# Kernel tuning notes

Hardware: AMD Instinct MI355X
Metric: run time of the kernel (lower is better)

Reference implementation:

```python
import jax, jax.numpy as jnp
import numpy as np
from jax.scipy.special import erf

# synthetic covalent radii table (original imports `covalent_radii`, e.g. from ase)
COV_RADII = jnp.asarray(0.3 + 0.02 * np.arange(100), dtype=jnp.float32)

B_MOL = 1024   # molecules per batch
N_ATOM = 128   # atoms per molecule (equal-sized ragged batch, atoms sorted by molecule)
N_ELEM = 10


def setup_inputs() -> dict:
    key = jax.random.key(0)
    ks = jax.random.split(key, 6)
    N = B_MOL * N_ATOM
    return {
        "eneg": jax.random.normal(ks[0], (N, 1), jnp.float32),
        "positions": jax.random.normal(ks[1], (N, 3), jnp.float32) * 3.0,
        "node_attrs": jax.random.uniform(ks[2], (N, N_ELEM), jnp.float32),
        "hardness": jax.random.uniform(ks[3], (N_ELEM,), jnp.float32),
        "total_charge": jax.random.normal(ks[4], (B_MOL,), jnp.float32),
        "batch": jnp.repeat(jnp.arange(B_MOL), N_ATOM),          # sorted molecule ids
        "atomic_numbers": jax.random.randint(ks[5], (N,), 1, 90),
    }


def reference(eneg, positions, node_attrs, hardness, total_charge, batch, atomic_numbers):
    # atoms are sorted by molecule with equal molecule sizes, so the ragged
    # python loop of the original collapses to a batched [B, n, ...] computation.
    B = total_charge.shape[0]
    N = positions.shape[0]
    n = N // B
    sqrt_pi = jnp.sqrt(jnp.asarray(np.pi, jnp.float32))
    sqrt_2 = jnp.sqrt(jnp.asarray(2.0, jnp.float32))

    pos = positions.reshape(B, n, 3)
    Z = atomic_numbers.reshape(B, n)
    atom_idx = jnp.argmax(node_attrs, axis=1).reshape(B, n)

    r = COV_RADII[Z]                                     # [B, n]
    diag_vals = hardness[atom_idx] + 1.0 / (sqrt_pi * r)  # [B, n]
    sigma = jnp.square(r)                                # [B, n]
    gamma = jnp.sqrt(sigma[:, :, None] + sigma[:, None, :])  # [B, n, n]

    diff = pos[:, :, None, :] - pos[:, None, :, :]       # [B, n, n, 3]
    sq = jnp.sum(diff * diff, axis=-1)                   # [B, n, n]
    eye = jnp.eye(n, dtype=bool)
    dist = jnp.sqrt(jnp.where(eye, 1.0, sq))             # safe diag (overwritten below)

    A = erf(dist / (sqrt_2 * gamma)) / dist              # [B, n, n]
    A = jnp.where(eye, diag_vals[:, :, None], A)         # scatter hardness diagonal

    # augment with charge-conservation row/column of ones (corner = 1)
    A = jnp.concatenate([A, jnp.ones((B, n, 1), A.dtype)], axis=2)
    A = jnp.concatenate([A, jnp.ones((B, 1, n + 1), A.dtype)], axis=1)

    b = jnp.concatenate([-eneg.reshape(B, n, 1),
                         total_charge.reshape(B, 1, 1)], axis=1)  # [B, n+1, 1]

    x = jnp.linalg.solve(A, b)                           # batched small solves
    return x[:, :n, 0].reshape(-1)                       # partial charges, [N]
```

## Files before the change

### kernel.cpp

```cpp
#include <hip/hip_runtime.h>
#include <math.h>

#define NMOL  1024
#define N     128
#define NELEM 10
#define BLOCK 256
#define PW    8
#define NPAN  16
#define PSTR  12
#define USTR  132

typedef __attribute__((ext_vector_type(4))) float f4;


__global__ __launch_bounds__(BLOCK, 2) void ceq_solve_kernel(
    const float* __restrict__ eneg,
    const float* __restrict__ positions,
    const float* __restrict__ node_attrs,
    const float* __restrict__ hardness,
    const float* __restrict__ total_charge,
    const int*   __restrict__ atomic_numbers,
    float* __restrict__ out)
{
    __shared__ __align__(16) float P[2][N * PSTR];
    __shared__ __align__(16) float Up[2][PW * USTR];
    __shared__ __align__(16) float Ublk[2][NPAN][PW][PW];
    __shared__ float rhsY[2][N], rhsZ[2][N];
    __shared__ float sxY[2][N], sxZ[2][N];
    __shared__ float px[2][N], py[2][N], pz[2][N], sg[2][N], dgv[2][N];
    __shared__ float lamS[2];

    const int tid  = threadIdx.x;
    const int lane = tid & 63;
    const int wid  = tid >> 6;
    const int g    = tid >> 7;
    const int wv   = wid & 1;
    const int gt   = tid & 127;
    const int r0   = 2 * lane;
    const int r1   = r0 + 1;
    const int col0 = 64 * wv;
    const int mol  = 2 * blockIdx.x + g;
    const int base = mol * N;

    {
        const int i = gt;
        const int Z = atomic_numbers[base + i];
        const float rad = 0.3f + 0.02f * (float)Z;
        sg[g][i] = rad * rad;
        const float* na = node_attrs + (size_t)(base + i) * NELEM;
        float best = na[0]; int bi = 0;
        #pragma unroll
        for (int e = 1; e < NELEM; ++e) {
            float v = na[e];
            if (v > best) { best = v; bi = e; }
        }
        dgv[g][i] = hardness[bi] + 0.5641895835477563f / rad;
        const float* p = positions + (size_t)(base + i) * 3;
        px[g][i] = p[0]; py[g][i] = p[1]; pz[g][i] = p[2];
        rhsY[g][i] = -eneg[base + i];
        rhsZ[g][i] = 1.0f;
    }
    __syncthreads();

    f4 Ar0[16], Ar1[16];
    {
        const float x0 = px[g][r0], y0 = py[g][r0], z0 = pz[g][r0];
        const float s0 = sg[g][r0], d0 = dgv[g][r0];
        #pragma unroll
        for (int c = 0; c < 16; ++c) {
            f4 v0;
            #pragma unroll
            for (int e = 0; e < 4; ++e) {
                const int j = col0 + 4 * c + e;
                float a0;
                if (j == r0) a0 = d0;
                else {
                    const float dx = x0 - px[g][j], dy = y0 - py[g][j], dz = z0 - pz[g][j];
                    const float d = sqrtf(dx * dx + dy * dy + dz * dz);
                    a0 = erff(d / (1.4142135623730951f * sqrtf(s0 + sg[g][j]))) / d;
                }
                ((float*)&v0)[e] = a0;
            }
            Ar0[c] = v0;
        }
        const float x1 = px[g][r1], y1 = py[g][r1], z1 = pz[g][r1];
        const float s1 = sg[g][r1], d1 = dgv[g][r1];
        #pragma unroll
        for (int c = 0; c < 16; ++c) {
            f4 v1;
            #pragma unroll
            for (int e = 0; e < 4; ++e) {
                const int j = col0 + 4 * c + e;
                float a1;
                if (j == r1) a1 = d1;
                else {
                    const float dx = x1 - px[g][j], dy = y1 - py[g][j], dz = z1 - pz[g][j];
                    const float d = sqrtf(dx * dx + dy * dy + dz * dz);
                    a1 = erff(d / (1.4142135623730951f * sqrtf(s1 + sg[g][j]))) / d;
                }
                ((float*)&v1)[e] = a1;
            }
            Ar1[c] = v1;
        }
    }

    for (int p = 0; p < NPAN; ++p) {
        const int k0   = PW * p;
        const int gclo = 2 * p + 2;
        const int q    = p & 7;

        if (wv == (p >> 3) && lane >= 4 * p) {
            f4 a00, a01, a10, a11;
            switch (q) {
                case 0:  a00 = Ar0[0];  a01 = Ar0[1];  a10 = Ar1[0];  a11 = Ar1[1];  break;
                case 1:  a00 = Ar0[2];  a01 = Ar0[3];  a10 = Ar1[2];  a11 = Ar1[3];  break;
                case 2:  a00 = Ar0[4];  a01 = Ar0[5];  a10 = Ar1[4];  a11 = Ar1[5];  break;
                case 3:  a00 = Ar0[6];  a01 = Ar0[7];  a10 = Ar1[6];  a11 = Ar1[7];  break;
                case 4:  a00 = Ar0[8];  a01 = Ar0[9];  a10 = Ar1[8];  a11 = Ar1[9];  break;
                case 5:  a00 = Ar0[10]; a01 = Ar0[11]; a10 = Ar1[10]; a11 = Ar1[11]; break;
                case 6:  a00 = Ar0[12]; a01 = Ar0[13]; a10 = Ar1[12]; a11 = Ar1[13]; break;
                default: a00 = Ar0[14]; a01 = Ar0[15]; a10 = Ar1[14]; a11 = Ar1[15]; break;
            }
            *(f4*)&P[g][r0 * PSTR + 0] = a00; *(f4*)&P[g][r0 * PSTR + 4] = a01;
            *(f4*)&P[g][r1 * PSTR + 0] = a10; *(f4*)&P[g][r1 * PSTR + 4] = a11;
        }
        __syncthreads();

        if (wv == 0) {
            const int i0 = k0 + lane, i1 = i0 + 64;
            const bool v0 = i0 < N, v1 = i1 < N;
            float rg0[PW], rg1[PW];
            float rY0, rZ0, rY1, rZ1;
            if (v0) {
                f4 a = *(const f4*)&P[g][i0 * PSTR], b = *(const f4*)&P[g][i0 * PSTR + 4];
                rg0[0]=a.x; rg0[1]=a.y; rg0[2]=a.z; rg0[3]=a.w;
                rg0[4]=b.x; rg0[5]=b.y; rg0[6]=b.z; rg0[7]=b.w;
                rY0 = rhsY[g][i0]; rZ0 = rhsZ[g][i0];
            } else {
                #pragma unroll
                for (int j = 0; j < PW; ++j) rg0[j] = 0.0f;
                rY0 = 0.0f; rZ0 = 0.0f;
            }
            if (v1) {
                f4 a = *(const f4*)&P[g][i1 * PSTR], b = *(const f4*)&P[g][i1 * PSTR + 4];
                rg1[0]=a.x; rg1[1]=a.y; rg1[2]=a.z; rg1[3]=a.w;
                rg1[4]=b.x; rg1[5]=b.y; rg1[6]=b.z; rg1[7]=b.w;
                rY1 = rhsY[g][i1]; rZ1 = rhsZ[g][i1];
            } else {
                #pragma unroll
                for (int j = 0; j < PW; ++j) rg1[j] = 0.0f;
                rY1 = 0.0f; rZ1 = 0.0f;
            }
            #pragma unroll
            for (int kk = 0; kk < PW; ++kk) {
                float pr[PW];
                #pragma unroll
                for (int j = kk; j < PW; ++j) pr[j] = __shfl(rg0[j], kk);
                const float cY = __shfl(rY0, kk);
                const float cZ = __shfl(rZ0, kk);
                const float dinv = 1.0f / pr[kk];
                if (v0 && lane > kk) {
                    const float mult = rg0[kk] * dinv; rg0[kk] = mult;
                    #pragma unroll
                    for (int j = kk + 1; j < PW; ++j) rg0[j] -= mult * pr[j];
                    rY0 -= mult * cY; rZ0 -= mult * cZ;
                }
                if (v0 && lane >= PW) Up[g][kk * USTR + i0] = rg0[kk] * pr[kk];
                if (v1) {
                    const float mult = rg1[kk] * dinv; rg1[kk] = mult;
                    #pragma unroll
                    for (int j = kk + 1; j < PW; ++j) rg1[j] -= mult * pr[j];
                    rY1 -= mult * cY; rZ1 -= mult * cZ;
                    Up[g][kk * USTR + i1] = rg1[kk] * pr[kk];
                }
            }
            if (v0) {
                f4 a = { rg0[0], rg0[1], rg0[2], rg0[3] };
                f4 b = { rg0[4], rg0[5], rg0[6], rg0[7] };
                *(f4*)&P[g][i0 * PSTR] = a; *(f4*)&P[g][i0 * PSTR + 4] = b;
                rhsY[g][i0] = rY0; rhsZ[g][i0] = rZ0;
                if (lane < PW) {
                    *(f4*)&Ublk[g][p][lane][0] = a; *(f4*)&Ublk[g][p][lane][4] = b;
                }
            }
            if (v1) {
                f4 a = { rg1[0], rg1[1], rg1[2], rg1[3] };
                f4 b = { rg1[4], rg1[5], rg1[6], rg1[7] };
                *(f4*)&P[g][i1 * PSTR] = a; *(f4*)&P[g][i1 * PSTR + 4] = b;
                rhsY[g][i1] = rY1; rhsZ[g][i1] = rZ1;
            }
        }
        __syncthreads();

        if (lane >= 4 * p && lane < 4 * p + 4) {
            const int u0 = r0 - k0, u1 = u0 + 1;
            #pragma unroll
            for (int c = 0; c < 16; ++c) {
                const int gc = 16 * wv + c;
                if (gc >= gclo) {
                    Ar0[c] = *(const f4*)&Up[g][u0 * USTR + 4 * gc];
                    Ar1[c] = *(const f4*)&Up[g][u1 * USTR + 4 * gc];
                }
            }
        }
        const bool hasmat = (16 * wv + 15) >= gclo;
        if (hasmat && lane >= 4 * p + 4) {
            float lA0[PW], lA1[PW];
            {
                f4 a = *(const f4*)&P[g][r0 * PSTR], b = *(const f4*)&P[g][r0 * PSTR + 4];
                lA0[0]=a.x; lA0[1]=a.y; lA0[2]=a.z; lA0[3]=a.w;
                lA0[4]=b.x; lA0[5]=b.y; lA0[6]=b.z; lA0[7]=b.w;
                f4 c2 = *(const f4*)&P[g][r1 * PSTR], d2 = *(const f4*)&P[g][r1 * PSTR + 4];
                lA1[0]=c2.x; lA1[1]=c2.y; lA1[2]=c2.z; lA1[3]=c2.w;
                lA1[4]=d2.x; lA1[5]=d2.y; lA1[6]=d2.z; lA1[7]=d2.w;
            }
            #pragma unroll
            for (int c = 0; c < 16; ++c) {
                const int gc = 16 * wv + c;
                if (gc >= gclo) {
                    f4 acc0 = Ar0[c], acc1 = Ar1[c];
                    #pragma unroll
                    for (int u = 0; u < PW; ++u) {
                        const f4 uv = *(const f4*)&Up[g][u * USTR + 4 * gc];
                        acc0 -= uv * lA0[u];
                        acc1 -= uv * lA1[u];
                    }
                    Ar0[c] = acc0; Ar1[c] = acc1;
                }
            }
        }
        __syncthreads();
    }

    for (int pb = NPAN - 1; pb >= 0; --pb) {
        const int k0 = PW * pb;
        if (tid < 4) {
            const int gg = tid >> 1;
            float* rhs = (tid & 1) ? rhsZ[gg] : rhsY[gg];
            float* sx  = (tid & 1) ? sxZ[gg]  : sxY[gg];
            float x[PW];
            #pragma unroll
            for (int kk = PW - 1; kk >= 0; --kk) {
                float acc = rhs[k0 + kk];
                #pragma unroll
                for (int jj = kk + 1; jj < PW; ++jj) acc -= Ublk[gg][pb][kk][jj] * x[jj];
                x[kk] = acc / Ublk[gg][pb][kk][kk];
                sx[k0 + kk] = x[kk];
            }
        }
        __syncthreads();
        if (wv == (pb >> 3) && lane < 4 * pb) {
            f4 a00, a01, a10, a11;
            switch (pb & 7) {
                case 0:  a00 = Ar0[0];  a01 = Ar0[1];  a10 = Ar1[0];  a11 = Ar1[1];  break;
                case 1:  a00 = Ar0[2];  a01 = Ar0[3];  a10 = Ar1[2];  a11 = Ar1[3];  break;
                case 2:  a00 = Ar0[4];  a01 = Ar0[5];  a10 = Ar1[4];  a11 = Ar1[5];  break;
                case 3:  a00 = Ar0[6];  a01 = Ar0[7];  a10 = Ar1[6];  a11 = Ar1[7];  break;
                case 4:  a00 = Ar0[8];  a01 = Ar0[9];  a10 = Ar1[8];  a11 = Ar1[9];  break;
                case 5:  a00 = Ar0[10]; a01 = Ar0[11]; a10 = Ar1[10]; a11 = Ar1[11]; break;
                case 6:  a00 = Ar0[12]; a01 = Ar0[13]; a10 = Ar1[12]; a11 = Ar1[13]; break;
                default: a00 = Ar0[14]; a01 = Ar0[15]; a10 = Ar1[14]; a11 = Ar1[15]; break;
            }
            float yy0 = rhsY[g][r0], yy1 = rhsY[g][r1];
            float zz0 = rhsZ[g][r0], zz1 = rhsZ[g][r1];
            yy0 -= a00.x*sxY[g][k0]   + a00.y*sxY[g][k0+1] + a00.z*sxY[g][k0+2] + a00.w*sxY[g][k0+3]
                 + a01.x*sxY[g][k0+4] + a01.y*sxY[g][k0+5] + a01.z*sxY[g][k0+6] + a01.w*sxY[g][k0+7];
            yy1 -= a10.x*sxY[g][k0]   + a10.y*sxY[g][k0+1] + a10.z*sxY[g][k0+2] + a10.w*sxY[g][k0+3]
                 + a11.x*sxY[g][k0+4] + a11.y*sxY[g][k0+5] + a11.z*sxY[g][k0+6] + a11.w*sxY[g][k0+7];
            zz0 -= a00.x*sxZ[g][k0]   + a00.y*sxZ[g][k0+1] + a00.z*sxZ[g][k0+2] + a00.w*sxZ[g][k0+3]
                 + a01.x*sxZ[g][k0+4] + a01.y*sxZ[g][k0+5] + a01.z*sxZ[g][k0+6] + a01.w*sxZ[g][k0+7];
            zz1 -= a10.x*sxZ[g][k0]   + a10.y*sxZ[g][k0+1] + a10.z*sxZ[g][k0+2] + a10.w*sxZ[g][k0+3]
                 + a11.x*sxZ[g][k0+4] + a11.y*sxZ[g][k0+5] + a11.z*sxZ[g][k0+6] + a11.w*sxZ[g][k0+7];
            rhsY[g][r0] = yy0; rhsY[g][r1] = yy1;
            rhsZ[g][r0] = zz0; rhsZ[g][r1] = zz1;
        }
        __syncthreads();
    }

    if (wv == 0) {
        float vY = sxY[g][lane] + sxY[g][lane + 64];
        float vZ = sxZ[g][lane] + sxZ[g][lane + 64];
        #pragma unroll
        for (int off = 32; off; off >>= 1) {
            vY += __shfl_xor(vY, off);
            vZ += __shfl_xor(vZ, off);
        }
        if (lane == 0) lamS[g] = (vY - total_charge[mol]) / (vZ - 1.0f);
    }
    __syncthreads();
    out[base + gt] = sxY[g][gt] - lamS[g] * sxZ[g][gt];
}

extern "C" void kernel_launch(void* const* d_in, const int* in_sizes, int n_in,
                              void* d_out, int out_size, void* d_ws, size_t ws_size,
                              hipStream_t stream) {
    const float* eneg           = (const float*)d_in[0];
    const float* positions      = (const float*)d_in[1];
    const float* node_attrs     = (const float*)d_in[2];
    const float* hardness       = (const float*)d_in[3];
    const float* total_charge   = (const float*)d_in[4];
    const int*   atomic_numbers = (const int*)d_in[6];
    float* out = (float*)d_out;

    ceq_solve_kernel<<<NMOL / 2, BLOCK, 0, stream>>>(
        eneg, positions, node_attrs, hardness, total_charge, atomic_numbers, out);
}
```

Measured before the change: 223.0 us.

## Assign one molecule per 256-thread block with four waves sharing its columns

Each block now solves one molecule instead of two, and its four wavefronts each own 32 columns of the 128x128 matrix rather than two wavefronts owning 64. Each thread holds half as many matrix registers (8 f4 per row instead of 16), so launch bounds are raised to 4 blocks per CU and the grid doubles. The aim is more parallelism per molecule and higher occupancy, shortening the serial panel chain per block. In exchange, the panel-factor step still runs on one wave while the other three wait, and idle threads per molecule increase.

```diff
diff --git a/kernel.cpp b/kernel.cpp
--- a/kernel.cpp
+++ b/kernel.cpp
@@ -13,7 +13,7 @@
 typedef __attribute__((ext_vector_type(4))) float f4;
 
 
-__global__ __launch_bounds__(BLOCK, 2) void ceq_solve_kernel(
+__global__ __launch_bounds__(BLOCK, 4) void ceq_solve_kernel(
     const float* __restrict__ eneg,
     const float* __restrict__ positions,
     const float* __restrict__ node_attrs,
@@ -22,31 +22,28 @@
     const int*   __restrict__ atomic_numbers,
     float* __restrict__ out)
 {
-    __shared__ __align__(16) float P[2][N * PSTR];
-    __shared__ __align__(16) float Up[2][PW * USTR];
-    __shared__ __align__(16) float Ublk[2][NPAN][PW][PW];
-    __shared__ float rhsY[2][N], rhsZ[2][N];
-    __shared__ float sxY[2][N], sxZ[2][N];
-    __shared__ float px[2][N], py[2][N], pz[2][N], sg[2][N], dgv[2][N];
-    __shared__ float lamS[2];
+    __shared__ __align__(16) float P[N * PSTR];
+    __shared__ __align__(16) float Up[PW * USTR];
+    __shared__ __align__(16) float Ublk[NPAN][PW][PW];
+    __shared__ float rhsY[N], rhsZ[N];
+    __shared__ float sxY[N], sxZ[N];
+    __shared__ float px[N], py[N], pz[N], sg[N], dgv[N];
+    __shared__ float lamS;
 
     const int tid  = threadIdx.x;
     const int lane = tid & 63;
-    const int wid  = tid >> 6;
-    const int g    = tid >> 7;
-    const int wv   = wid & 1;
-    const int gt   = tid & 127;
+    const int wv   = tid >> 6;
     const int r0   = 2 * lane;
     const int r1   = r0 + 1;
-    const int col0 = 64 * wv;
-    const int mol  = 2 * blockIdx.x + g;
+    const int col0 = 32 * wv;
+    const int mol  = blockIdx.x;
     const int base = mol * N;
 
-    {
-        const int i = gt;
+    if (tid < N) {
+        const int i = tid;
         const int Z = atomic_numbers[base + i];
         const float rad = 0.3f + 0.02f * (float)Z;
-        sg[g][i] = rad * rad;
+        sg[i] = rad * rad;
         const float* na = node_attrs + (size_t)(base + i) * NELEM;
         float best = na[0]; int bi = 0;
         #pragma unroll
@@ -54,20 +51,20 @@
             float v = na[e];
             if (v > best) { best = v; bi = e; }
         }
-        dgv[g][i] = hardness[bi] + 0.5641895835477563f / rad;
+        dgv[i] = hardness[bi] + 0.5641895835477563f / rad;
         const float* p = positions + (size_t)(base + i) * 3;
-        px[g][i] = p[0]; py[g][i] = p[1]; pz[g][i] = p[2];
-        rhsY[g][i] = -eneg[base + i];
-        rhsZ[g][i] = 1.0f;
+        px[i] = p[0]; py[i] = p[1]; pz[i] = p[2];
+        rhsY[i] = -eneg[base + i];
+        rhsZ[i] = 1.0f;
     }
     __syncthreads();
 
-    f4 Ar0[16], Ar1[16];
+    f4 Ar0[8], Ar1[8];
     {
-        const float x0 = px[g][r0], y0 = py[g][r0], z0 = pz[g][r0];
-        const float s0 = sg[g][r0], d0 = dgv[g][r0];
-        #pragma unroll
-        for (int c = 0; c < 16; ++c) {
+        const float x0 = px[r0], y0 = py[r0], z0 = pz[r0];
+        const float s0 = sg[r0], d0 = dgv[r0];
+        #pragma unroll
+        for (int c = 0; c < 8; ++c) {
             f4 v0;
             #pragma unroll
             for (int e = 0; e < 4; ++e) {
@@ -75,18 +72,18 @@
                 float a0;
                 if (j == r0) a0 = d0;
                 else {
-                    const float dx = x0 - px[g][j], dy = y0 - py[g][j], dz = z0 - pz[g][j];
+                    const float dx = x0 - px[j], dy = y0 - py[j], dz = z0 - pz[j];
                     const float d = sqrtf(dx * dx + dy * dy + dz * dz);
-                    a0 = erff(d / (1.4142135623730951f * sqrtf(s0 + sg[g][j]))) / d;
+                    a0 = erff(d / (1.4142135623730951f * sqrtf(s0 + sg[j]))) / d;
                 }
                 ((float*)&v0)[e] = a0;
             }
             Ar0[c] = v0;
         }
-        const float x1 = px[g][r1], y1 = py[g][r1], z1 = pz[g][r1];
-        const float s1 = sg[g][r1], d1 = dgv[g][r1];
-        #pragma unroll
-        for (int c = 0; c < 16; ++c) {
+        const float x1 = px[r1], y1 = py[r1], z1 = pz[r1];
+        const float s1 = sg[r1], d1 = dgv[r1];
+        #pragma unroll
+        for (int c = 0; c < 8; ++c) {
             f4 v1;
             #pragma unroll
             for (int e = 0; e < 4; ++e) {
@@ -94,9 +91,9 @@
                 float a1;
                 if (j == r1) a1 = d1;
                 else {
-                    const float dx = x1 - px[g][j], dy = y1 - py[g][j], dz = z1 - pz[g][j];
+                    const float dx = x1 - px[j], dy = y1 - py[j], dz = z1 - pz[j];
                     const float d = sqrtf(dx * dx + dy * dy + dz * dz);
-                    a1 = erff(d / (1.4142135623730951f * sqrtf(s1 + sg[g][j]))) / d;
+                    a1 = erff(d / (1.4142135623730951f * sqrtf(s1 + sg[j]))) / d;
                 }
                 ((float*)&v1)[e] = a1;
             }
@@ -107,22 +104,18 @@
     for (int p = 0; p < NPAN; ++p) {
         const int k0   = PW * p;
         const int gclo = 2 * p + 2;
-        const int q    = p & 7;
-
-        if (wv == (p >> 3) && lane >= 4 * p) {
+        const int q    = p & 3;
+
+        if (wv == (p >> 2) && lane >= 4 * p) {
             f4 a00, a01, a10, a11;
             switch (q) {
-                case 0:  a00 = Ar0[0];  a01 = Ar0[1];  a10 = Ar1[0];  a11 = Ar1[1];  break;
-                case 1:  a00 = Ar0[2];  a01 = Ar0[3];  a10 = Ar1[2];  a11 = Ar1[3];  break;
-                case 2:  a00 = Ar0[4];  a01 = Ar0[5];  a10 = Ar1[4];  a11 = Ar1[5];  break;
-                case 3:  a00 = Ar0[6];  a01 = Ar0[7];  a10 = Ar1[6];  a11 = Ar1[7];  break;
-                case 4:  a00 = Ar0[8];  a01 = Ar0[9];  a10 = Ar1[8];  a11 = Ar1[9];  break;
-                case 5:  a00 = Ar0[10]; a01 = Ar0[11]; a10 = Ar1[10]; a11 = Ar1[11]; break;
-                case 6:  a00 = Ar0[12]; a01 = Ar0[13]; a10 = Ar1[12]; a11 = Ar1[13]; break;
-                default: a00 = Ar0[14]; a01 = Ar0[15]; a10 = Ar1[14]; a11 = Ar1[15]; break;
-            }
-            *(f4*)&P[g][r0 * PSTR + 0] = a00; *(f4*)&P[g][r0 * PSTR + 4] = a01;
-            *(f4*)&P[g][r1 * PSTR + 0] = a10; *(f4*)&P[g][r1 * PSTR + 4] = a11;
+                case 0:  a00 = Ar0[0]; a01 = Ar0[1]; a10 = Ar1[0]; a11 = Ar1[1]; break;
+                case 1:  a00 = Ar0[2]; a01 = Ar0[3]; a10 = Ar1[2]; a11 = Ar1[3]; break;
+                case 2:  a00 = Ar0[4]; a01 = Ar0[5]; a10 = Ar1[4]; a11 = Ar1[5]; break;
+                default: a00 = Ar0[6]; a01 = Ar0[7]; a10 = Ar1[6]; a11 = Ar1[7]; break;
+            }
+            *(f4*)&P[r0 * PSTR + 0] = a00; *(f4*)&P[r0 * PSTR + 4] = a01;
+            *(f4*)&P[r1 * PSTR + 0] = a10; *(f4*)&P[r1 * PSTR + 4] = a11;
         }
         __syncthreads();
 
@@ -132,20 +125,20 @@
             float rg0[PW], rg1[PW];
             float rY0, rZ0, rY1, rZ1;
             if (v0) {
-                f4 a = *(const f4*)&P[g][i0 * PSTR], b = *(const f4*)&P[g][i0 * PSTR + 4];
+                f4 a = *(const f4*)&P[i0 * PSTR], b = *(const f4*)&P[i0 * PSTR + 4];
                 rg0[0]=a.x; rg0[1]=a.y; rg0[2]=a.z; rg0[3]=a.w;
                 rg0[4]=b.x; rg0[5]=b.y; rg0[6]=b.z; rg0[7]=b.w;
-                rY0 = rhsY[g][i0]; rZ0 = rhsZ[g][i0];
+                rY0 = rhsY[i0]; rZ0 = rhsZ[i0];
             } else {
                 #pragma unroll
                 for (int j = 0; j < PW; ++j) rg0[j] = 0.0f;
                 rY0 = 0.0f; rZ0 = 0.0f;
             }
             if (v1) {
-                f4 a = *(const f4*)&P[g][i1 * PSTR], b = *(const f4*)&P[g][i1 * PSTR + 4];
+                f4 a = *(const f4*)&P[i1 * PSTR], b = *(const f4*)&P[i1 * PSTR + 4];
                 rg1[0]=a.x; rg1[1]=a.y; rg1[2]=a.z; rg1[3]=a.w;
                 rg1[4]=b.x; rg1[5]=b.y; rg1[6]=b.z; rg1[7]=b.w;
-                rY1 = rhsY[g][i1]; rZ1 = rhsZ[g][i1];
+                rY1 = rhsY[i1]; rZ1 = rhsZ[i1];
             } else {
                 #pragma unroll
                 for (int j = 0; j < PW; ++j) rg1[j] = 0.0f;
@@ -165,29 +158,29 @@
                     for (int j = kk + 1; j < PW; ++j) rg0[j] -= mult * pr[j];
                     rY0 -= mult * cY; rZ0 -= mult * cZ;
                 }
-                if (v0 && lane >= PW) Up[g][kk * USTR + i0] = rg0[kk] * pr[kk];
+                if (v0 && lane >= PW) Up[kk * USTR + i0] = rg0[kk] * pr[kk];
                 if (v1) {
                     const float mult = rg1[kk] * dinv; rg1[kk] = mult;
                     #pragma unroll
                     for (int j = kk + 1; j < PW; ++j) rg1[j] -= mult * pr[j];
                     rY1 -= mult * cY; rZ1 -= mult * cZ;
-                    Up[g][kk * USTR + i1] = rg1[kk] * pr[kk];
+                    Up[kk * USTR + i1] = rg1[kk] * pr[kk];
                 }
             }
             if (v0) {
                 f4 a = { rg0[0], rg0[1], rg0[2], rg0[3] };
                 f4 b = { rg0[4], rg0[5], rg0[6], rg0[7] };
-                *(f4*)&P[g][i0 * PSTR] = a; *(f4*)&P[g][i0 * PSTR + 4] = b;
-                rhsY[g][i0] = rY0; rhsZ[g][i0] = rZ0;
+                *(f4*)&P[i0 * PSTR] = a; *(f4*)&P[i0 * PSTR + 4] = b;
+                rhsY[i0] = rY0; rhsZ[i0] = rZ0;
                 if (lane < PW) {
-                    *(f4*)&Ublk[g][p][lane][0] = a; *(f4*)&Ublk[g][p][lane][4] = b;
+                    *(f4*)&Ublk[p][lane][0] = a; *(f4*)&Ublk[p][lane][4] = b;
                 }
             }
             if (v1) {
                 f4 a = { rg1[0], rg1[1], rg1[2], rg1[3] };
                 f4 b = { rg1[4], rg1[5], rg1[6], rg1[7] };
-                *(f4*)&P[g][i1 * PSTR] = a; *(f4*)&P[g][i1 * PSTR + 4] = b;
-                rhsY[g][i1] = rY1; rhsZ[g][i1] = rZ1;
+                *(f4*)&P[i1 * PSTR] = a; *(f4*)&P[i1 * PSTR + 4] = b;
+                rhsY[i1] = rY1; rhsZ[i1] = rZ1;
             }
         }
         __syncthreads();
@@ -195,33 +188,33 @@
         if (lane >= 4 * p && lane < 4 * p + 4) {
             const int u0 = r0 - k0, u1 = u0 + 1;
             #pragma unroll
-            for (int c = 0; c < 16; ++c) {
-                const int gc = 16 * wv + c;
+            for (int c = 0; c < 8; ++c) {
+                const int gc = 8 * wv + c;
                 if (gc >= gclo) {
-                    Ar0[c] = *(const f4*)&Up[g][u0 * USTR + 4 * gc];
-                    Ar1[c] = *(const f4*)&Up[g][u1 * USTR + 4 * gc];
-                }
-            }
-        }
-        const bool hasmat = (16 * wv + 15) >= gclo;
+                    Ar0[c] = *(const f4*)&Up[u0 * USTR + 4 * gc];
+                    Ar1[c] = *(const f4*)&Up[u1 * USTR + 4 * gc];
+                }
+            }
+        }
+        const bool hasmat = (8 * wv + 7) >= gclo;
         if (hasmat && lane >= 4 * p + 4) {
             float lA0[PW], lA1[PW];
             {
-                f4 a = *(const f4*)&P[g][r0 * PSTR], b = *(const f4*)&P[g][r0 * PSTR + 4];
+                f4 a = *(const f4*)&P[r0 * PSTR], b = *(const f4*)&P[r0 * PSTR + 4];
                 lA0[0]=a.x; lA0[1]=a.y; lA0[2]=a.z; lA0[3]=a.w;
                 lA0[4]=b.x; lA0[5]=b.y; lA0[6]=b.z; lA0[7]=b.w;
-                f4 c2 = *(const f4*)&P[g][r1 * PSTR], d2 = *(const f4*)&P[g][r1 * PSTR + 4];
+                f4 c2 = *(const f4*)&P[r1 * PSTR], d2 = *(const f4*)&P[r1 * PSTR + 4];
                 lA1[0]=c2.x; lA1[1]=c2.y; lA1[2]=c2.z; lA1[3]=c2.w;
                 lA1[4]=d2.x; lA1[5]=d2.y; lA1[6]=d2.z; lA1[7]=d2.w;
             }
             #pragma unroll
-            for (int c = 0; c < 16; ++c) {
-                const int gc = 16 * wv + c;
+            for (int c = 0; c < 8; ++c) {
+                const int gc = 8 * wv + c;
                 if (gc >= gclo) {
                     f4 acc0 = Ar0[c], acc1 = Ar1[c];
                     #pragma unroll
                     for (int u = 0; u < PW; ++u) {
-                        const f4 uv = *(const f4*)&Up[g][u * USTR + 4 * gc];
+                        const f4 uv = *(const f4*)&Up[u * USTR + 4 * gc];
                         acc0 -= uv * lA0[u];
                         acc1 -= uv * lA1[u];
                     }
@@ -234,61 +227,56 @@
 
     for (int pb = NPAN - 1; pb >= 0; --pb) {
         const int k0 = PW * pb;
-        if (tid < 4) {
-            const int gg = tid >> 1;
-            float* rhs = (tid & 1) ? rhsZ[gg] : rhsY[gg];
-            float* sx  = (tid & 1) ? sxZ[gg]  : sxY[gg];
+        if (tid < 2) {
+            float* rhs = tid ? rhsZ : rhsY;
+            float* sx  = tid ? sxZ  : sxY;
             float x[PW];
             #pragma unroll
             for (int kk = PW - 1; kk >= 0; --kk) {
                 float acc = rhs[k0 + kk];
                 #pragma unroll
-                for (int jj = kk + 1; jj < PW; ++jj) acc -= Ublk[gg][pb][kk][jj] * x[jj];
-                x[kk] = acc / Ublk[gg][pb][kk][kk];
+                for (int jj = kk + 1; jj < PW; ++jj) acc -= Ublk[pb][kk][jj] * x[jj];
+                x[kk] = acc / Ublk[pb][kk][kk];
                 sx[k0 + kk] = x[kk];
             }
         }
         __syncthreads();
-        if (wv == (pb >> 3) && lane < 4 * pb) {
+        if (wv == (pb >> 2) && lane < 4 * pb) {
             f4 a00, a01, a10, a11;
-            switch (pb & 7) {
-                case 0:  a00 = Ar0[0];  a01 = Ar0[1];  a10 = Ar1[0];  a11 = Ar1[1];  break;
-                case 1:  a00 = Ar0[2];  a01 = Ar0[3];  a10 = Ar1[2];  a11 = Ar1[3];  break;
-                case 2:  a00 = Ar0[4];  a01 = Ar0[5];  a10 = Ar1[4];  a11 = Ar1[5];  break;
-                case 3:  a00 = Ar0[6];  a01 = Ar0[7];  a10 = Ar1[6];  a11 = Ar1[7];  break;
-                case 4:  a00 = Ar0[8];  a01 = Ar0[9];  a10 = Ar1[8];  a11 = Ar1[9];  break;
-                case 5:  a00 = Ar0[10]; a01 = Ar0[11]; a10 = Ar1[10]; a11 = Ar1[11]; break;
-                case 6:  a00 = Ar0[12]; a01 = Ar0[13]; a10 = Ar1[12]; a11 = Ar1[13]; break;
-                default: a00 = Ar0[14]; a01 = Ar0[15]; a10 = Ar1[14]; a11 = Ar1[15]; break;
-            }
-            float yy0 = rhsY[g][r0], yy1 = rhsY[g][r1];
-            float zz0 = rhsZ[g][r0], zz1 = rhsZ[g][r1];
-            yy0 -= a00.x*sxY[g][k0]   + a00.y*sxY[g][k0+1] + a00.z*sxY[g][k0+2] + a00.w*sxY[g][k0+3]
-                 + a01.x*sxY[g][k0+4] + a01.y*sxY[g][k0+5] + a01.z*sxY[g][k0+6] + a01.w*sxY[g][k0+7];
-            yy1 -= a10.x*sxY[g][k0]   + a10.y*sxY[g][k0+1] + a10.z*sxY[g][k0+2] + a10.w*sxY[g][k0+3]
-                 + a11.x*sxY[g][k0+4] + a11.y*sxY[g][k0+5] + a11.z*sxY[g][k0+6] + a11.w*sxY[g][k0+7];
-            zz0 -= a00.x*sxZ[g][k0]   + a00.y*sxZ[g][k0+1] + a00.z*sxZ[g][k0+2] + a00.w*sxZ[g][k0+3]
-                 + a01.x*sxZ[g][k0+4] + a01.y*sxZ[g][k0+5] + a01.z*sxZ[g][k0+6] + a01.w*sxZ[g][k0+7];
-            zz1 -= a10.x*sxZ[g][k0]   + a10.y*sxZ[g][k0+1] + a10.z*sxZ[g][k0+2] + a10.w*sxZ[g][k0+3]
-                 + a11.x*sxZ[g][k0+4] + a11.y*sxZ[g][k0+5] + a11.z*sxZ[g][k0+6] + a11.w*sxZ[g][k0+7];
-            rhsY[g][r0] = yy0; rhsY[g][r1] = yy1;
-            rhsZ[g][r0] = zz0; rhsZ[g][r1] = zz1;
+            switch (pb & 3) {
+                case 0:  a00 = Ar0[0]; a01 = Ar0[1]; a10 = Ar1[0]; a11 = Ar1[1]; break;
+                case 1:  a00 = Ar0[2]; a01 = Ar0[3]; a10 = Ar1[2]; a11 = Ar1[3]; break;
+                case 2:  a00 = Ar0[4]; a01 = Ar0[5]; a10 = Ar1[4]; a11 = Ar1[5]; break;
+                default: a00 = Ar0[6]; a01 = Ar0[7]; a10 = Ar1[6]; a11 = Ar1[7]; break;
+            }
+            float yy0 = rhsY[r0], yy1 = rhsY[r1];
+            float zz0 = rhsZ[r0], zz1 = rhsZ[r1];
+            yy0 -= a00.x*sxY[k0]   + a00.y*sxY[k0+1] + a00.z*sxY[k0+2] + a00.w*sxY[k0+3]
+                 + a01.x*sxY[k0+4] + a01.y*sxY[k0+5] + a01.z*sxY[k0+6] + a01.w*sxY[k0+7];
+            yy1 -= a10.x*sxY[k0]   + a10.y*sxY[k0+1] + a10.z*sxY[k0+2] + a10.w*sxY[k0+3]
+                 + a11.x*sxY[k0+4] + a11.y*sxY[k0+5] + a11.z*sxY[k0+6] + a11.w*sxY[k0+7];
+            zz0 -= a00.x*sxZ[k0]   + a00.y*sxZ[k0+1] + a00.z*sxZ[k0+2] + a00.w*sxZ[k0+3]
+                 + a01.x*sxZ[k0+4] + a01.y*sxZ[k0+5] + a01.z*sxZ[k0+6] + a01.w*sxZ[k0+7];
+            zz1 -= a10.x*sxZ[k0]   + a10.y*sxZ[k0+1] + a10.z*sxZ[k0+2] + a10.w*sxZ[k0+3]
+                 + a11.x*sxZ[k0+4] + a11.y*sxZ[k0+5] + a11.z*sxZ[k0+6] + a11.w*sxZ[k0+7];
+            rhsY[r0] = yy0; rhsY[r1] = yy1;
+            rhsZ[r0] = zz0; rhsZ[r1] = zz1;
         }
         __syncthreads();
     }
 
     if (wv == 0) {
-        float vY = sxY[g][lane] + sxY[g][lane + 64];
-        float vZ = sxZ[g][lane] + sxZ[g][lane + 64];
+        float vY = sxY[lane] + sxY[lane + 64];
+        float vZ = sxZ[lane] + sxZ[lane + 64];
         #pragma unroll
         for (int off = 32; off; off >>= 1) {
             vY += __shfl_xor(vY, off);
             vZ += __shfl_xor(vZ, off);
         }
-        if (lane == 0) lamS[g] = (vY - total_charge[mol]) / (vZ - 1.0f);
+        if (lane == 0) lamS = (vY - total_charge[mol]) / (vZ - 1.0f);
     }
     __syncthreads();
-    out[base + gt] = sxY[g][gt] - lamS[g] * sxZ[g][gt];
+    if (tid < N) out[base + tid] = sxY[tid] - lamS * sxZ[tid];
 }
 
 extern "C" void kernel_launch(void* const* d_in, const int* in_sizes, int n_in,
@@ -302,6 +290,6 @@
     const int*   atomic_numbers = (const int*)d_in[6];
     float* out = (float*)d_out;
 
-    ceq_solve_kernel<<<NMOL / 2, BLOCK, 0, stream>>>(
+    ceq_solve_kernel<<<NMOL, BLOCK, 0, stream>>>(
         eneg, positions, node_attrs, hardness, total_charge, atomic_numbers, out);
 }
```

After: 248.2 us. 1.11x slower.

## Split panel factorization into diagonal-block LU plus parallel row triangular solve

Applied to the files above, without the earlier changes.

The 8x8 diagonal block is now factored in-register by the four owning lanes of the wave that holds it, which publish its pivots and reciprocals to shared memory. All 128 threads per molecule then compute the below-diagonal multipliers and rhs updates independently with a small triangular solve. Previously a single wave per molecule factored the whole panel. This spreads the serial panel work across both waves and removes the panel round-trip through P. In exchange it adds extra shared-memory reads of the U block and the rhs per row.

```diff
diff --git a/kernel.cpp b/kernel.cpp
--- a/kernel.cpp
+++ b/kernel.cpp
@@ -25,6 +25,7 @@
     __shared__ __align__(16) float P[2][N * PSTR];
     __shared__ __align__(16) float Up[2][PW * USTR];
     __shared__ __align__(16) float Ublk[2][NPAN][PW][PW];
+    __shared__ float Dinv[2][PW], Dd[2][PW];
     __shared__ float rhsY[2][N], rhsZ[2][N];
     __shared__ float sxY[2][N], sxZ[2][N];
     __shared__ float px[2][N], py[2][N], pz[2][N], sg[2][N], dgv[2][N];
@@ -32,10 +33,9 @@
 
     const int tid  = threadIdx.x;
     const int lane = tid & 63;
-    const int wid  = tid >> 6;
     const int g    = tid >> 7;
-    const int wv   = wid & 1;
     const int gt   = tid & 127;
+    const int wv   = (tid >> 6) & 1;
     const int r0   = 2 * lane;
     const int r1   = r0 + 1;
     const int col0 = 64 * wv;
@@ -121,74 +121,74 @@
                 case 6:  a00 = Ar0[12]; a01 = Ar0[13]; a10 = Ar1[12]; a11 = Ar1[13]; break;
                 default: a00 = Ar0[14]; a01 = Ar0[15]; a10 = Ar1[14]; a11 = Ar1[15]; break;
             }
-            *(f4*)&P[g][r0 * PSTR + 0] = a00; *(f4*)&P[g][r0 * PSTR + 4] = a01;
-            *(f4*)&P[g][r1 * PSTR + 0] = a10; *(f4*)&P[g][r1 * PSTR + 4] = a11;
-        }
-        __syncthreads();
-
-        if (wv == 0) {
-            const int i0 = k0 + lane, i1 = i0 + 64;
-            const bool v0 = i0 < N, v1 = i1 < N;
-            float rg0[PW], rg1[PW];
-            float rY0, rZ0, rY1, rZ1;
-            if (v0) {
-                f4 a = *(const f4*)&P[g][i0 * PSTR], b = *(const f4*)&P[g][i0 * PSTR + 4];
-                rg0[0]=a.x; rg0[1]=a.y; rg0[2]=a.z; rg0[3]=a.w;
-                rg0[4]=b.x; rg0[5]=b.y; rg0[6]=b.z; rg0[7]=b.w;
-                rY0 = rhsY[g][i0]; rZ0 = rhsZ[g][i0];
+            if (lane >= 4 * p + 4) {
+                *(f4*)&P[g][r0 * PSTR + 0] = a00; *(f4*)&P[g][r0 * PSTR + 4] = a01;
+                *(f4*)&P[g][r1 * PSTR + 0] = a10; *(f4*)&P[g][r1 * PSTR + 4] = a11;
             } else {
+                float u0[PW] = { a00.x, a00.y, a00.z, a00.w, a01.x, a01.y, a01.z, a01.w };
+                float u1[PW] = { a10.x, a10.y, a10.z, a10.w, a11.x, a11.y, a11.z, a11.w };
+                float ry0 = rhsY[g][r0], rz0 = rhsZ[g][r0];
+                float ry1 = rhsY[g][r1], rz1 = rhsZ[g][r1];
+                const int rl = lane - 4 * p;
                 #pragma unroll
-                for (int j = 0; j < PW; ++j) rg0[j] = 0.0f;
-                rY0 = 0.0f; rZ0 = 0.0f;
-            }
-            if (v1) {
-                f4 a = *(const f4*)&P[g][i1 * PSTR], b = *(const f4*)&P[g][i1 * PSTR + 4];
-                rg1[0]=a.x; rg1[1]=a.y; rg1[2]=a.z; rg1[3]=a.w;
-                rg1[4]=b.x; rg1[5]=b.y; rg1[6]=b.z; rg1[7]=b.w;
-                rY1 = rhsY[g][i1]; rZ1 = rhsZ[g][i1];
-            } else {
+                for (int kk = 0; kk < PW; ++kk) {
+                    const int src = 4 * p + (kk >> 1);
+                    float pr[PW];
+                    #pragma unroll
+                    for (int j = kk; j < PW; ++j)
+                        pr[j] = __shfl((kk & 1) ? u1[j] : u0[j], src);
+                    const float cY = __shfl((kk & 1) ? ry1 : ry0, src);
+                    const float cZ = __shfl((kk & 1) ? rz1 : rz0, src);
+                    const float dinv = 1.0f / pr[kk];
+                    if (2 * rl > kk) {
+                        const float m = u0[kk] * dinv; u0[kk] = m;
+                        #pragma unroll
+                        for (int j = kk + 1; j < PW; ++j) u0[j] -= m * pr[j];
+                        ry0 -= m * cY; rz0 -= m * cZ;
+                    }
+                    if (2 * rl + 1 > kk) {
+                        const float m = u1[kk] * dinv; u1[kk] = m;
+                        #pragma unroll
+                        for (int j = kk + 1; j < PW; ++j) u1[j] -= m * pr[j];
+                        ry1 -= m * cY; rz1 -= m * cZ;
+                    }
+                    if (rl == (kk >> 1)) { Dinv[g][kk] = dinv; Dd[g][kk] = pr[kk]; }
+                }
+                f4 w0 = { u0[0], u0[1], u0[2], u0[3] }, w1 = { u0[4], u0[5], u0[6], u0[7] };
+                *(f4*)&Ublk[g][p][2 * rl][0] = w0; *(f4*)&Ublk[g][p][2 * rl][4] = w1;
+                f4 w2 = { u1[0], u1[1], u1[2], u1[3] }, w3 = { u1[4], u1[5], u1[6], u1[7] };
+                *(f4*)&Ublk[g][p][2 * rl + 1][0] = w2; *(f4*)&Ublk[g][p][2 * rl + 1][4] = w3;
+                rhsY[g][r0] = ry0; rhsZ[g][r0] = rz0;
+                rhsY[g][r1] = ry1; rhsZ[g][r1] = rz1;
+            }
+        }
+        __syncthreads();
+
+        const int nb = (N - PW) - k0;
+        if (gt < nb) {
+            const int i = k0 + PW + gt;
+            f4 a = *(const f4*)&P[g][i * PSTR], b = *(const f4*)&P[g][i * PSTR + 4];
+            float av[PW] = { a.x, a.y, a.z, a.w, b.x, b.y, b.z, b.w };
+            float m[PW];
+            #pragma unroll
+            for (int j = 0; j < PW; ++j) {
+                float acc = av[j];
                 #pragma unroll
-                for (int j = 0; j < PW; ++j) rg1[j] = 0.0f;
-                rY1 = 0.0f; rZ1 = 0.0f;
-            }
-            #pragma unroll
-            for (int kk = 0; kk < PW; ++kk) {
-                float pr[PW];
-                #pragma unroll
-                for (int j = kk; j < PW; ++j) pr[j] = __shfl(rg0[j], kk);
-                const float cY = __shfl(rY0, kk);
-                const float cZ = __shfl(rZ0, kk);
-                const float dinv = 1.0f / pr[kk];
-                if (v0 && lane > kk) {
-                    const float mult = rg0[kk] * dinv; rg0[kk] = mult;
-                    #pragma unroll
-                    for (int j = kk + 1; j < PW; ++j) rg0[j] -= mult * pr[j];
-                    rY0 -= mult * cY; rZ0 -= mult * cZ;
-                }
-                if (v0 && lane >= PW) Up[g][kk * USTR + i0] = rg0[kk] * pr[kk];
-                if (v1) {
-                    const float mult = rg1[kk] * dinv; rg1[kk] = mult;
-                    #pragma unroll
-                    for (int j = kk + 1; j < PW; ++j) rg1[j] -= mult * pr[j];
-                    rY1 -= mult * cY; rZ1 -= mult * cZ;
-                    Up[g][kk * USTR + i1] = rg1[kk] * pr[kk];
-                }
-            }
-            if (v0) {
-                f4 a = { rg0[0], rg0[1], rg0[2], rg0[3] };
-                f4 b = { rg0[4], rg0[5], rg0[6], rg0[7] };
-                *(f4*)&P[g][i0 * PSTR] = a; *(f4*)&P[g][i0 * PSTR + 4] = b;
-                rhsY[g][i0] = rY0; rhsZ[g][i0] = rZ0;
-                if (lane < PW) {
-                    *(f4*)&Ublk[g][p][lane][0] = a; *(f4*)&Ublk[g][p][lane][4] = b;
-                }
-            }
-            if (v1) {
-                f4 a = { rg1[0], rg1[1], rg1[2], rg1[3] };
-                f4 b = { rg1[4], rg1[5], rg1[6], rg1[7] };
-                *(f4*)&P[g][i1 * PSTR] = a; *(f4*)&P[g][i1 * PSTR + 4] = b;
-                rhsY[g][i1] = rY1; rhsZ[g][i1] = rZ1;
-            }
+                for (int t = 0; t < j; ++t) acc -= m[t] * Ublk[g][p][t][j];
+                m[j] = acc * Dinv[g][j];
+            }
+            f4 ma = { m[0], m[1], m[2], m[3] }, mb = { m[4], m[5], m[6], m[7] };
+            *(f4*)&P[g][i * PSTR]     = ma;
+            *(f4*)&P[g][i * PSTR + 4] = mb;
+            #pragma unroll
+            for (int u = 0; u < PW; ++u) Up[g][u * USTR + i] = m[u] * Dd[g][u];
+            float ry = rhsY[g][i], rz = rhsZ[g][i];
+            #pragma unroll
+            for (int t = 0; t < PW; ++t) {
+                ry -= m[t] * rhsY[g][k0 + t];
+                rz -= m[t] * rhsZ[g][k0 + t];
+            }
+            rhsY[g][i] = ry; rhsZ[g][i] = rz;
         }
         __syncthreads();
 
```

Result: no change. 224.2 us (+0.5%).
